# Kernel tuning notes

Hardware: AMD Instinct MI355X
Metric: run time of the kernel (lower is better)

Reference implementation:

```python
import jax, jax.numpy as jnp
import numpy as np

DN = ('NWC', 'WIO', 'NWC')  # Keras Conv1D layout: x=[B,T,C], w=[k,Cin,Cout]


def causal_conv(x, w, b, dilation):
    k = w.shape[0]
    pad = (k - 1) * dilation
    xp = jnp.pad(x, ((0, 0), (pad, 0), (0, 0)))
    y = jax.lax.conv_general_dilated(xp, w, window_strides=(1,), padding='VALID',
                                     rhs_dilation=(dilation,), dimension_numbers=DN)
    return jax.nn.relu(y + b)


def setup_inputs() -> dict:
    key = jax.random.key(0)
    ks = jax.random.split(key, 20)
    B, T, Cin, F = 32, 4096, 192, 320
    cb, cl = F // 5, F - 4 * (F // 5)  # 64, 64
    s = 0.05
    inp = {
        'x': jax.random.normal(ks[0], (B, T, Cin), jnp.float32),
        'w_b1': jax.random.normal(ks[1], (3, Cin, cb), jnp.float32) * s,
        'b_b1': jax.random.normal(ks[2], (cb,), jnp.float32) * s,
        'w_b2': jax.random.normal(ks[3], (3, Cin, cb), jnp.float32) * s,
        'b_b2': jax.random.normal(ks[4], (cb,), jnp.float32) * s,
        'w_b3': jax.random.normal(ks[5], (5, Cin, cb), jnp.float32) * s,
        'b_b3': jax.random.normal(ks[6], (cb,), jnp.float32) * s,
        'w_b4': jax.random.normal(ks[7], (9, Cin, cb), jnp.float32) * s,
        'b_b4': jax.random.normal(ks[8], (cb,), jnp.float32) * s,
        'w_b5': jax.random.normal(ks[9], (9, Cin, cl), jnp.float32) * s,
        'b_b5': jax.random.normal(ks[10], (cl,), jnp.float32) * s,
        'w_att1': jax.random.normal(ks[11], (F, F // 4), jnp.float32) * s,
        'b_att1': jax.random.normal(ks[12], (F // 4,), jnp.float32) * s,
        'w_att2': jax.random.normal(ks[13], (F // 4, F), jnp.float32) * s,
        'b_att2': jax.random.normal(ks[14], (F,), jnp.float32) * s,
        'w_out': jax.random.normal(ks[15], (1, F, F), jnp.float32) * s,
        'b_out': jax.random.normal(ks[16], (F,), jnp.float32) * s,
    }
    return inp


def reference(x, w_b1, b_b1, w_b2, b_b2, w_b3, b_b3, w_b4, b_b4, w_b5, b_b5,
              w_att1, b_att1, w_att2, b_att2, w_out, b_out):
    # multi-scale causal dilated branches (sequence-processing path)
    x1 = causal_conv(x, w_b1, b_b1, 1)
    x2 = causal_conv(x, w_b2, b_b2, 2)
    x3 = causal_conv(x, w_b3, b_b3, 4)
    x4 = causal_conv(x, w_b4, b_b4, 8)
    x5 = causal_conv(x, w_b5, b_b5, 12)
    xc = jnp.concatenate([x1, x2, x3, x4, x5], axis=-1)  # [B,T,F]
    # SE-style per-timestep gating
    att = jax.nn.relu(jnp.einsum('btf,fh->bth', xc, w_att1) + b_att1)
    att = jax.nn.sigmoid(jnp.einsum('bth,hf->btf', att, w_att2) + b_att2)
    xa = xc * att
    # 1x1 conv out == matmul over channel dim
    return jnp.einsum('btf,fg->btg', xa, w_out[0]) + b_out
```

## Files before the change

### kernel.cpp

```cpp
#include <hip/hip_runtime.h>

typedef __attribute__((ext_vector_type(8))) short short8;
typedef __attribute__((ext_vector_type(16))) float f32x16;
typedef __attribute__((ext_vector_type(4))) unsigned short us4;

#define MFMA32(a,b,c) __builtin_amdgcn_mfma_f32_32x32x16_bf16((a),(b),(c),0,0,0)

__device__ __forceinline__ unsigned short f2bf(float f) {
  union { float f; unsigned u; } v; v.f = f;
  return (unsigned short)((v.u + 0x7fffu + ((v.u >> 16) & 1u)) >> 16);
}
__device__ __forceinline__ float bf2f(unsigned short h) {
  union { unsigned u; float f; } v; v.u = ((unsigned)h) << 16;
  return v.f;
}
__device__ __forceinline__ f32x16 zero16() {
  f32x16 v;
  #pragma unroll
  for (int i = 0; i < 16; ++i) v[i] = 0.f;
  return v;
}

__global__ __launch_bounds__(256) void k_prep(
    const float* __restrict__ w1, const float* __restrict__ w2,
    const float* __restrict__ w3, const float* __restrict__ w4,
    const float* __restrict__ w5,
    const float* __restrict__ b1, const float* __restrict__ b2,
    const float* __restrict__ b3, const float* __restrict__ b4,
    const float* __restrict__ b5,
    const float* __restrict__ wa1, const float* __restrict__ wa2,
    const float* __restrict__ wo,
    unsigned short* __restrict__ wtcf, unsigned short* __restrict__ w1f,
    unsigned short* __restrict__ w2f, unsigned short* __restrict__ wof,
    float* __restrict__ bcat)
{
  int i = blockIdx.x * 256 + threadIdx.x;
  if (i < 356352) {
    int e = i & 7, l = (i >> 3) & 63, ks = (i >> 9) % 12;
    int rest = i / 6144; int nt2 = rest & 1, t = rest >> 1;
    int k = ks * 16 + (l >> 5) * 8 + e;
    int n = nt2 * 32 + (l & 31);
    const float* w; int j;
    if (t < 3)       { w = w1; j = t; }
    else if (t < 6)  { w = w2; j = t - 3; }
    else if (t < 11) { w = w3; j = t - 6; }
    else if (t < 20) { w = w4; j = t - 11; }
    else             { w = w5; j = t - 20; }
    wtcf[i] = f2bf(w[(j * 192 + k) * 64 + n]);
    return;
  }
  i -= 356352;
  if (i < 30720) {
    int e = i & 7, l = (i >> 3) & 63, ks = (i >> 9) % 20, nt = i / 10240;
    int h = nt * 32 + (l & 31), k = ks * 16 + (l >> 5) * 8 + e;
    w1f[i] = (h < 80) ? f2bf(wa1[k * 80 + h]) : (unsigned short)0;
    return;
  }
  i -= 30720;
  if (i < 30720) {
    int e = i & 7, l = (i >> 3) & 63, ks = (i >> 9) % 6, nt = i / 3072;
    int f = nt * 32 + (l & 31), k = ks * 16 + (l >> 5) * 8 + e;
    w2f[i] = (k < 80) ? f2bf(wa2[k * 320 + f]) : (unsigned short)0;
    return;
  }
  i -= 30720;
  if (i < 102400) {
    int e = i & 7, l = (i >> 3) & 63, ks = (i >> 9) % 20, nt = i / 10240;
    int g = nt * 32 + (l & 31), k = ks * 16 + (l >> 5) * 8 + e;
    wof[i] = f2bf(wo[k * 320 + g]);
    return;
  }
  i -= 102400;
  if (i < 320) {
    float v;
    if (i < 64)       v = b1[i];
    else if (i < 128) v = b2[i - 64];
    else if (i < 192) v = b3[i - 128];
    else if (i < 256) v = b4[i - 192];
    else              v = b5[i - 256];
    bcat[i] = v;
  }
}

#define XS_STRIDE 400
#define XCB_OFF   64000
#define LDS_TOTAL (64000 + 40960)

template<int KT, int DL, int TB>
__device__ __forceinline__ void conv_unit(
    const unsigned char* __restrict__ smem,
    unsigned char* __restrict__ xcb,
    const unsigned short* __restrict__ wtcf,
    const float* __restrict__ bcat,
    int br, int mt, int l31, int lh, int lane)
{
  f32x16 a0e = zero16(), a0o = zero16(), a1e = zero16(), a1o = zero16();
  const int arow0 = 96 + mt * 32 + l31;
  #pragma unroll
  for (int j = 0; j < KT; ++j) {
    const int roff = arow0 - DL * (KT - 1 - j);
    const unsigned char* xr = smem + roff * XS_STRIDE + lh * 16;
    const unsigned short* wp0 = wtcf + (size_t)((TB + j) * 2 + 0) * 6144 + lane * 8;
    const unsigned short* wp1 = wp0 + 6144;
    #pragma unroll
    for (int ks = 0; ks < 12; ks += 2) {
      short8 be0 = *(const short8*)(wp0 + ks * 512);
      short8 be1 = *(const short8*)(wp1 + ks * 512);
      short8 ae  = *(const short8*)(xr + ks * 32);
      a0e = MFMA32(ae, be0, a0e);
      a1e = MFMA32(ae, be1, a1e);
      short8 bo0 = *(const short8*)(wp0 + ks * 512 + 512);
      short8 bo1 = *(const short8*)(wp1 + ks * 512 + 512);
      short8 ao  = *(const short8*)(xr + ks * 32 + 32);
      a0o = MFMA32(ao, bo0, a0o);
      a1o = MFMA32(ao, bo1, a1o);
    }
  }
  #pragma unroll
  for (int nh = 0; nh < 2; ++nh) {
    const int col = (br * 2 + nh) * 32 + l31;
    const float bias = bcat[col];
    #pragma unroll
    for (int r = 0; r < 16; ++r) {
      int row = mt * 32 + (r & 3) + 8 * (r >> 2) + 4 * lh;
      float v = (nh ? (a1e[r] + a1o[r]) : (a0e[r] + a0o[r])) + bias;
      v = v > 0.f ? v : 0.f;
      *(unsigned short*)(xcb + row * 640 + ((2 * col) ^ ((row & 7) << 4))) = f2bf(v);
    }
  }
}

__global__ __launch_bounds__(512, 2) void k_fused(
    const float* __restrict__ x, const unsigned short* __restrict__ wtcf,
    const unsigned short* __restrict__ w1f, const unsigned short* __restrict__ w2f,
    const unsigned short* __restrict__ wof, const float* __restrict__ bcat,
    const float* __restrict__ ba1, const float* __restrict__ ba2,
    const float* __restrict__ bo, float* __restrict__ out)
{
  __shared__ __align__(16) unsigned char smem[LDS_TOTAL];
  unsigned char* xcb = smem + XCB_OFF;
  unsigned char* a1b = smem;

  int bid = blockIdx.x;
  bid = (bid & 7) * 256 + (bid >> 3);
  const int m0 = bid * 64;
  const int b  = m0 >> 12;
  const int t0 = m0 & 4095;
  const int tid = threadIdx.x;
  const int wid = tid >> 6, lane = tid & 63;
  const int l31 = lane & 31, lh = lane >> 5;
  const int sw = (l31 & 7) << 4;

  const float* xb = x + (size_t)b * 4096 * 192;
  #pragma unroll
  for (int it = 0; it < 15; ++it) {
    int c = tid + it * 512;
    int r = c / 48, f = c - r * 48;
    int tp = t0 - 96 + r;
    float4 v = make_float4(0.f, 0.f, 0.f, 0.f);
    if (tp >= 0) v = *(const float4*)(xb + (size_t)tp * 192 + f * 4);
    us4 o = { f2bf(v.x), f2bf(v.y), f2bf(v.z), f2bf(v.w) };
    *(us4*)(smem + r * XS_STRIDE + f * 8) = o;
  }
  __syncthreads();

  {
    const int mt = wid & 1;
    switch (wid >> 1) {
      case 0: conv_unit<9,12,20>(smem, xcb, wtcf, bcat, 4, mt, l31, lh, lane); break;
      case 1: conv_unit<9, 8,11>(smem, xcb, wtcf, bcat, 3, mt, l31, lh, lane); break;
      case 2: conv_unit<5, 4, 6>(smem, xcb, wtcf, bcat, 2, mt, l31, lh, lane); break;
      default:
        conv_unit<3, 2, 3>(smem, xcb, wtcf, bcat, 1, mt, l31, lh, lane);
        conv_unit<3, 1, 0>(smem, xcb, wtcf, bcat, 0, mt, l31, lh, lane);
        break;
    }
  }
  __syncthreads();

  if (wid < 6) {
    const int mt = wid & 1, nt1 = wid >> 1;
    const int arow = mt * 32 + l31;
    f32x16 acc = zero16();
    const unsigned short* bp = w1f + (size_t)(nt1 * 20) * 512 + lane * 8;
    #pragma unroll
    for (int ks = 0; ks < 20; ++ks) {
      short8 af = *(const short8*)(xcb + arow * 640 + ((ks * 32 + lh * 16) ^ sw));
      short8 bf = *(const short8*)(bp + ks * 512);
      acc = MFMA32(af, bf, acc);
    }
    const int h = nt1 * 32 + l31;
    const float bias = (h < 80) ? ba1[h] : 0.f;
    #pragma unroll
    for (int r = 0; r < 16; ++r) {
      int row = mt * 32 + (r & 3) + 8 * (r >> 2) + 4 * lh;
      float v = acc[r] + bias;
      v = v > 0.f ? v : 0.f;
      *(unsigned short*)(a1b + row * 256 + ((2 * h) ^ ((row & 7) << 4))) = f2bf(v);
    }
  }
  __syncthreads();

  const int mt2 = wid & 1, g = wid >> 1;
  const int tcount = (g < 2) ? 3 : 2;
  const int tbase  = (g < 2) ? g * 3 : 6 + (g - 2) * 2;
  const int arow2 = mt2 * 32 + l31;
  {
    f32x16 acc2[3];
    #pragma unroll
    for (int t = 0; t < 3; ++t) acc2[t] = zero16();
    #pragma unroll
    for (int ks = 0; ks < 6; ++ks) {
      short8 af = *(const short8*)(a1b + arow2 * 256 + ((ks * 32 + lh * 16) ^ sw));
      #pragma unroll
      for (int t = 0; t < 3; ++t) if (t < tcount) {
        short8 bf = *(const short8*)(w2f + (size_t)((tbase + t) * 6 + ks) * 512 + lane * 8);
        acc2[t] = MFMA32(af, bf, acc2[t]);
      }
    }
    #pragma unroll
    for (int t = 0; t < 3; ++t) if (t < tcount) {
      const int col = (tbase + t) * 32 + l31;
      const float bias = ba2[col];
      #pragma unroll
      for (int r = 0; r < 16; ++r) {
        int row = mt2 * 32 + (r & 3) + 8 * (r >> 2) + 4 * lh;
        float v = acc2[t][r] + bias;
        float s = 1.f / (1.f + __expf(-v));
        unsigned short* p =
            (unsigned short*)(xcb + row * 640 + ((2 * col) ^ ((row & 7) << 4)));
        *p = f2bf(bf2f(*p) * s);
      }
    }
  }
  __syncthreads();

  {
    f32x16 acc4[3];
    #pragma unroll
    for (int t = 0; t < 3; ++t) acc4[t] = zero16();
    #pragma unroll
    for (int ks = 0; ks < 20; ++ks) {
      short8 af = *(const short8*)(xcb + arow2 * 640 + ((ks * 32 + lh * 16) ^ sw));
      #pragma unroll
      for (int t = 0; t < 3; ++t) if (t < tcount) {
        short8 bf = *(const short8*)(wof + (size_t)((tbase + t) * 20 + ks) * 512 + lane * 8);
        acc4[t] = MFMA32(af, bf, acc4[t]);
      }
    }
    #pragma unroll
    for (int t = 0; t < 3; ++t) if (t < tcount) {
      const int col = (tbase + t) * 32 + l31;
      const float bias = bo[col];
      #pragma unroll
      for (int r = 0; r < 16; ++r) {
        int row = mt2 * 32 + (r & 3) + 8 * (r >> 2) + 4 * lh;
        out[(size_t)(m0 + row) * 320 + col] = acc4[t][r] + bias;
      }
    }
  }
}

extern "C" void kernel_launch(void* const* d_in, const int* in_sizes, int n_in,
                              void* d_out, int out_size, void* d_ws, size_t ws_size,
                              hipStream_t stream) {
  const float* x    = (const float*)d_in[0];
  const float* w_b1 = (const float*)d_in[1];  const float* b_b1 = (const float*)d_in[2];
  const float* w_b2 = (const float*)d_in[3];  const float* b_b2 = (const float*)d_in[4];
  const float* w_b3 = (const float*)d_in[5];  const float* b_b3 = (const float*)d_in[6];
  const float* w_b4 = (const float*)d_in[7];  const float* b_b4 = (const float*)d_in[8];
  const float* w_b5 = (const float*)d_in[9];  const float* b_b5 = (const float*)d_in[10];
  const float* wa1  = (const float*)d_in[11]; const float* ba1  = (const float*)d_in[12];
  const float* wa2  = (const float*)d_in[13]; const float* ba2  = (const float*)d_in[14];
  const float* wo   = (const float*)d_in[15]; const float* bo   = (const float*)d_in[16];

  char* ws = (char*)d_ws;
  unsigned short* wtcf = (unsigned short*)(ws);
  unsigned short* w1f  = (unsigned short*)(ws + 712704);
  unsigned short* w2f  = (unsigned short*)(ws + 774144);
  unsigned short* wof  = (unsigned short*)(ws + 835584);
  float*          bct  = (float*)         (ws + 1040384);

  k_prep<<<2034, 256, 0, stream>>>(w_b1, w_b2, w_b3, w_b4, w_b5,
                                   b_b1, b_b2, b_b3, b_b4, b_b5,
                                   wa1, wa2, wo, wtcf, w1f, w2f, wof, bct);
  k_fused<<<2048, 512, 0, stream>>>(x, wtcf, w1f, w2f, wof, bct,
                                    ba1, ba2, bo, (float*)d_out);
}
```

Before: 576.8 us.

## Split fused kernel into conv and gating/output kernels with 128-row tiles

Replaces the single fused kernel with two kernels. The first computes the five causal conv branches over 128-timestep tiles and writes the bf16 concatenated activations into the output buffer as scratch. The second stages that data into LDS with global_load_lds and then runs the SE gating and the output projection in place. Larger tiles shrink the relative halo cost and let each weight fragment feed two MFMAs, and the split frees LDS per stage. In exchange it adds a global round trip for the intermediate, and at 1024 threads per block with large LDS footprints occupancy is likely low.

Measured after the change: 492.9 us. -14.6%, faster.

```diff
diff --git a/kernel.cpp b/kernel.cpp
--- a/kernel.cpp
+++ b/kernel.cpp
@@ -19,6 +19,11 @@
   #pragma unroll
   for (int i = 0; i < 16; ++i) v[i] = 0.f;
   return v;
+}
+__device__ __forceinline__ void gload16(const void* g, void* l) {
+  __builtin_amdgcn_global_load_lds(
+      (const __attribute__((address_space(1))) void*)(g),
+      (__attribute__((address_space(3))) void*)(l), 16, 0, 0);
 }
 
 __global__ __launch_bounds__(256) void k_prep(
@@ -82,180 +87,183 @@
   }
 }
 
-#define XS_STRIDE 400
-#define XCB_OFF   64000
-#define LDS_TOTAL (64000 + 40960)
-
 template<int KT, int DL, int TB>
 __device__ __forceinline__ void conv_unit(
-    const unsigned char* __restrict__ smem,
-    unsigned char* __restrict__ xcb,
-    const unsigned short* __restrict__ wtcf,
-    const float* __restrict__ bcat,
-    int br, int mt, int l31, int lh, int lane)
-{
-  f32x16 a0e = zero16(), a0o = zero16(), a1e = zero16(), a1o = zero16();
-  const int arow0 = 96 + mt * 32 + l31;
+    const unsigned char* smem, const unsigned short* __restrict__ wtcf,
+    const float* __restrict__ bcat, unsigned char* __restrict__ xcg,
+    int nh, int p, int br, int l31, int lh, int lane)
+{
+  f32x16 acc0 = zero16(), acc1 = zero16();
+  const int r0 = 96 + p * 64 + l31;
   #pragma unroll
   for (int j = 0; j < KT; ++j) {
-    const int roff = arow0 - DL * (KT - 1 - j);
-    const unsigned char* xr = smem + roff * XS_STRIDE + lh * 16;
-    const unsigned short* wp0 = wtcf + (size_t)((TB + j) * 2 + 0) * 6144 + lane * 8;
-    const unsigned short* wp1 = wp0 + 6144;
-    #pragma unroll
-    for (int ks = 0; ks < 12; ks += 2) {
-      short8 be0 = *(const short8*)(wp0 + ks * 512);
-      short8 be1 = *(const short8*)(wp1 + ks * 512);
-      short8 ae  = *(const short8*)(xr + ks * 32);
-      a0e = MFMA32(ae, be0, a0e);
-      a1e = MFMA32(ae, be1, a1e);
-      short8 bo0 = *(const short8*)(wp0 + ks * 512 + 512);
-      short8 bo1 = *(const short8*)(wp1 + ks * 512 + 512);
-      short8 ao  = *(const short8*)(xr + ks * 32 + 32);
-      a0o = MFMA32(ao, bo0, a0o);
-      a1o = MFMA32(ao, bo1, a1o);
-    }
-  }
-  #pragma unroll
-  for (int nh = 0; nh < 2; ++nh) {
-    const int col = (br * 2 + nh) * 32 + l31;
-    const float bias = bcat[col];
+    const int row = r0 - DL * (KT - 1 - j);
+    const int sw = (row & 15) << 4;
+    const unsigned char* x0 = smem + row * 512;
+    const unsigned short* wp =
+        wtcf + (size_t)(((TB + j) * 2 + nh) * 12) * 512 + lane * 8;
+    #pragma unroll
+    for (int ks = 0; ks < 12; ++ks) {
+      const int cb = (ks * 32 + lh * 16) ^ sw;
+      short8 bf = *(const short8*)(wp + ks * 512);
+      short8 a0 = *(const short8*)(x0 + cb);
+      short8 a1 = *(const short8*)(x0 + 32 * 512 + cb);
+      acc0 = MFMA32(a0, bf, acc0);
+      acc1 = MFMA32(a1, bf, acc1);
+    }
+  }
+  const int col = (br * 2 + nh) * 32 + l31;
+  const float bias = bcat[col];
+  #pragma unroll
+  for (int h = 0; h < 2; ++h) {
+    const f32x16& A = h ? acc1 : acc0;
     #pragma unroll
     for (int r = 0; r < 16; ++r) {
-      int row = mt * 32 + (r & 3) + 8 * (r >> 2) + 4 * lh;
-      float v = (nh ? (a1e[r] + a1o[r]) : (a0e[r] + a0o[r])) + bias;
-      v = v > 0.f ? v : 0.f;
-      *(unsigned short*)(xcb + row * 640 + ((2 * col) ^ ((row & 7) << 4))) = f2bf(v);
-    }
-  }
-}
-
-__global__ __launch_bounds__(512, 2) void k_fused(
+      int row = p * 64 + h * 32 + (r & 3) + 8 * (r >> 2) + 4 * lh;
+      float v = A[r] + bias; v = v > 0.f ? v : 0.f;
+      *(unsigned short*)(xcg + (size_t)row * 768 +
+                         ((2 * col) ^ ((row & 15) << 4))) = f2bf(v);
+    }
+  }
+}
+
+__global__ __launch_bounds__(1024, 4) void k_fconv(
     const float* __restrict__ x, const unsigned short* __restrict__ wtcf,
-    const unsigned short* __restrict__ w1f, const unsigned short* __restrict__ w2f,
-    const unsigned short* __restrict__ wof, const float* __restrict__ bcat,
-    const float* __restrict__ ba1, const float* __restrict__ ba2,
-    const float* __restrict__ bo, float* __restrict__ out)
-{
-  __shared__ __align__(16) unsigned char smem[LDS_TOTAL];
-  unsigned char* xcb = smem + XCB_OFF;
-  unsigned char* a1b = smem;
-
+    const float* __restrict__ bcat, unsigned char* __restrict__ xcglob)
+{
+  __shared__ __align__(16) unsigned char smem[224 * 512];
   int bid = blockIdx.x;
-  bid = (bid & 7) * 256 + (bid >> 3);
-  const int m0 = bid * 64;
+  bid = (bid & 7) * 128 + (bid >> 3);
+  const int m0 = bid * 128;
   const int b  = m0 >> 12;
   const int t0 = m0 & 4095;
   const int tid = threadIdx.x;
+
+  const float* xb = x + (size_t)b * 4096 * 192;
+  #pragma unroll
+  for (int it = 0; it < 11; ++it) {
+    int c = tid + it * 1024;
+    if (c < 10752) {
+      int r = c / 48, f = c - r * 48;
+      int tp = t0 - 96 + r;
+      float4 v = make_float4(0.f, 0.f, 0.f, 0.f);
+      if (tp >= 0) v = *(const float4*)(xb + (size_t)tp * 192 + f * 4);
+      us4 o = { f2bf(v.x), f2bf(v.y), f2bf(v.z), f2bf(v.w) };
+      *(us4*)(smem + r * 512 + ((f * 8) ^ ((r & 15) << 4))) = o;
+    }
+  }
+  __syncthreads();
+
   const int wid = tid >> 6, lane = tid & 63;
   const int l31 = lane & 31, lh = lane >> 5;
-  const int sw = (l31 & 7) << 4;
-
-  const float* xb = x + (size_t)b * 4096 * 192;
-  #pragma unroll
-  for (int it = 0; it < 15; ++it) {
-    int c = tid + it * 512;
-    int r = c / 48, f = c - r * 48;
-    int tp = t0 - 96 + r;
-    float4 v = make_float4(0.f, 0.f, 0.f, 0.f);
-    if (tp >= 0) v = *(const float4*)(xb + (size_t)tp * 192 + f * 4);
-    us4 o = { f2bf(v.x), f2bf(v.y), f2bf(v.z), f2bf(v.w) };
-    *(us4*)(smem + r * XS_STRIDE + f * 8) = o;
-  }
-  __syncthreads();
+  unsigned char* xcg = xcglob + (size_t)m0 * 1280;
+
+  if (wid < 4)       conv_unit<9, 8,11>(smem, wtcf, bcat, xcg, (wid>>1)&1, wid&1, 3, l31, lh, lane);
+  else if (wid < 8)  conv_unit<9,12,20>(smem, wtcf, bcat, xcg, (wid>>1)&1, wid&1, 4, l31, lh, lane);
+  else if (wid < 12) conv_unit<5, 4, 6>(smem, wtcf, bcat, xcg, (wid>>1)&1, wid&1, 2, l31, lh, lane);
+  else if (wid < 14) {
+    conv_unit<3, 1, 0>(smem, wtcf, bcat, xcg, wid & 1, 0, 0, l31, lh, lane);
+    conv_unit<3, 1, 0>(smem, wtcf, bcat, xcg, wid & 1, 1, 0, l31, lh, lane);
+  } else {
+    conv_unit<3, 2, 3>(smem, wtcf, bcat, xcg, wid & 1, 0, 1, l31, lh, lane);
+    conv_unit<3, 2, 3>(smem, wtcf, bcat, xcg, wid & 1, 1, 1, l31, lh, lane);
+  }
+}
+
+__global__ __launch_bounds__(1024, 4) void k_gateout(
+    const unsigned char* __restrict__ xcglob,
+    const unsigned short* __restrict__ w1f, const unsigned short* __restrict__ w2f,
+    const unsigned short* __restrict__ wof,
+    const float* __restrict__ ba1, const float* __restrict__ ba2,
+    const float* __restrict__ bo, float* __restrict__ out)
+{
+  __shared__ __align__(16) unsigned char smem[128 * 768 + 128 * 256];
+  unsigned char* a1b = smem + 128 * 768;
+  int bid = blockIdx.x;
+  bid = (bid & 7) * 128 + (bid >> 3);
+  const int m0 = bid * 128;
+  const int tid = threadIdx.x;
+  const int wid = tid >> 6, lane = tid & 63;
+  const int l31 = lane & 31, lh = lane >> 5;
+  const int sw15 = (l31 & 15) << 4, sw7 = (l31 & 7) << 4;
 
   {
-    const int mt = wid & 1;
-    switch (wid >> 1) {
-      case 0: conv_unit<9,12,20>(smem, xcb, wtcf, bcat, 4, mt, l31, lh, lane); break;
-      case 1: conv_unit<9, 8,11>(smem, xcb, wtcf, bcat, 3, mt, l31, lh, lane); break;
-      case 2: conv_unit<5, 4, 6>(smem, xcb, wtcf, bcat, 2, mt, l31, lh, lane); break;
-      default:
-        conv_unit<3, 2, 3>(smem, xcb, wtcf, bcat, 1, mt, l31, lh, lane);
-        conv_unit<3, 1, 0>(smem, xcb, wtcf, bcat, 0, mt, l31, lh, lane);
-        break;
-    }
-  }
-  __syncthreads();
-
-  if (wid < 6) {
-    const int mt = wid & 1, nt1 = wid >> 1;
-    const int arow = mt * 32 + l31;
+    const unsigned char* src = xcglob + (size_t)m0 * 1280 + wid * 6144 + lane * 16;
+    unsigned char* dst = smem + wid * 6144;
+    #pragma unroll
+    for (int k = 0; k < 6; ++k)
+      gload16(src + k * 1024, dst + k * 1024);
+  }
+  __syncthreads();
+
+  if (wid < 12) {
+    const int nt = wid >> 2, mt = wid & 3;
     f32x16 acc = zero16();
-    const unsigned short* bp = w1f + (size_t)(nt1 * 20) * 512 + lane * 8;
+    const unsigned short* bp = w1f + (size_t)(nt * 20) * 512 + lane * 8;
+    const unsigned char* ar = smem + (size_t)(mt * 32 + l31) * 768;
     #pragma unroll
     for (int ks = 0; ks < 20; ++ks) {
-      short8 af = *(const short8*)(xcb + arow * 640 + ((ks * 32 + lh * 16) ^ sw));
+      short8 af = *(const short8*)(ar + ((ks * 32 + lh * 16) ^ sw15));
       short8 bf = *(const short8*)(bp + ks * 512);
       acc = MFMA32(af, bf, acc);
     }
-    const int h = nt1 * 32 + l31;
+    const int h = nt * 32 + l31;
     const float bias = (h < 80) ? ba1[h] : 0.f;
+    #pragma unroll
+    for (int r = 0; r < 16; ++r) {
+      int row = mt * 32 + (r & 3) + 8 * (r >> 2) + 4 * lh;
+      float v = acc[r] + bias; v = v > 0.f ? v : 0.f;
+      *(unsigned short*)(a1b + row * 256 + ((2 * h) ^ ((row & 7) << 4))) = f2bf(v);
+    }
+  }
+  __syncthreads();
+
+  for (int u = wid; u < 40; u += 16) {
+    const int col = u >> 2, mt = u & 3;
+    f32x16 acc = zero16();
+    const unsigned char* ar = a1b + (size_t)(mt * 32 + l31) * 256;
+    #pragma unroll
+    for (int ks = 0; ks < 6; ++ks) {
+      short8 af = *(const short8*)(ar + ((ks * 32 + lh * 16) ^ sw7));
+      short8 bf = *(const short8*)(w2f + (size_t)(col * 6 + ks) * 512 + lane * 8);
+      acc = MFMA32(af, bf, acc);
+    }
+    const float bias = ba2[col * 32 + l31];
     #pragma unroll
     for (int r = 0; r < 16; ++r) {
       int row = mt * 32 + (r & 3) + 8 * (r >> 2) + 4 * lh;
       float v = acc[r] + bias;
-      v = v > 0.f ? v : 0.f;
-      *(unsigned short*)(a1b + row * 256 + ((2 * h) ^ ((row & 7) << 4))) = f2bf(v);
-    }
-  }
-  __syncthreads();
-
-  const int mt2 = wid & 1, g = wid >> 1;
-  const int tcount = (g < 2) ? 3 : 2;
-  const int tbase  = (g < 2) ? g * 3 : 6 + (g - 2) * 2;
-  const int arow2 = mt2 * 32 + l31;
-  {
-    f32x16 acc2[3];
-    #pragma unroll
-    for (int t = 0; t < 3; ++t) acc2[t] = zero16();
-    #pragma unroll
-    for (int ks = 0; ks < 6; ++ks) {
-      short8 af = *(const short8*)(a1b + arow2 * 256 + ((ks * 32 + lh * 16) ^ sw));
-      #pragma unroll
-      for (int t = 0; t < 3; ++t) if (t < tcount) {
-        short8 bf = *(const short8*)(w2f + (size_t)((tbase + t) * 6 + ks) * 512 + lane * 8);
-        acc2[t] = MFMA32(af, bf, acc2[t]);
-      }
-    }
-    #pragma unroll
-    for (int t = 0; t < 3; ++t) if (t < tcount) {
-      const int col = (tbase + t) * 32 + l31;
-      const float bias = ba2[col];
+      float s = 1.f / (1.f + __expf(-v));
+      unsigned short* pp = (unsigned short*)(smem + (size_t)row * 768 +
+          ((2 * (col * 32 + l31)) ^ ((row & 15) << 4)));
+      *pp = f2bf(bf2f(*pp) * s);
+    }
+  }
+  __syncthreads();
+
+  for (int u = wid; u < 20; u += 16) {
+    const int col = u >> 1, p = u & 1;
+    f32x16 acc0 = zero16(), acc1 = zero16();
+    const unsigned char* ar0 = smem + (size_t)(p * 64 + l31) * 768;
+    const unsigned char* ar1 = ar0 + 32 * 768;
+    const unsigned short* bp = wof + (size_t)(col * 20) * 512 + lane * 8;
+    #pragma unroll
+    for (int ks = 0; ks < 20; ++ks) {
+      const int cb = (ks * 32 + lh * 16) ^ sw15;
+      short8 bf = *(const short8*)(bp + ks * 512);
+      short8 a0 = *(const short8*)(ar0 + cb);
+      short8 a1 = *(const short8*)(ar1 + cb);
+      acc0 = MFMA32(a0, bf, acc0);
+      acc1 = MFMA32(a1, bf, acc1);
+    }
+    const float bias = bo[col * 32 + l31];
+    #pragma unroll
+    for (int h = 0; h < 2; ++h) {
+      const f32x16& A = h ? acc1 : acc0;
       #pragma unroll
       for (int r = 0; r < 16; ++r) {
-        int row = mt2 * 32 + (r & 3) + 8 * (r >> 2) + 4 * lh;
-        float v = acc2[t][r] + bias;
-        float s = 1.f / (1.f + __expf(-v));
-        unsigned short* p =
-            (unsigned short*)(xcb + row * 640 + ((2 * col) ^ ((row & 7) << 4)));
-        *p = f2bf(bf2f(*p) * s);
-      }
-    }
-  }
-  __syncthreads();
-
-  {
-    f32x16 acc4[3];
-    #pragma unroll
-    for (int t = 0; t < 3; ++t) acc4[t] = zero16();
-    #pragma unroll
-    for (int ks = 0; ks < 20; ++ks) {
-      short8 af = *(const short8*)(xcb + arow2 * 640 + ((ks * 32 + lh * 16) ^ sw));
-      #pragma unroll
-      for (int t = 0; t < 3; ++t) if (t < tcount) {
-        short8 bf = *(const short8*)(wof + (size_t)((tbase + t) * 20 + ks) * 512 + lane * 8);
-        acc4[t] = MFMA32(af, bf, acc4[t]);
-      }
-    }
-    #pragma unroll
-    for (int t = 0; t < 3; ++t) if (t < tcount) {
-      const int col = (tbase + t) * 32 + l31;
-      const float bias = bo[col];
-      #pragma unroll
-      for (int r = 0; r < 16; ++r) {
-        int row = mt2 * 32 + (r & 3) + 8 * (r >> 2) + 4 * lh;
-        out[(size_t)(m0 + row) * 320 + col] = acc4[t][r] + bias;
+        int row = p * 64 + h * 32 + (r & 3) + 8 * (r >> 2) + 4 * lh;
+        out[(size_t)(m0 + row) * 320 + col * 32 + l31] = A[r] + bias;
       }
     }
   }
@@ -284,6 +292,8 @@
   k_prep<<<2034, 256, 0, stream>>>(w_b1, w_b2, w_b3, w_b4, w_b5,
                                    b_b1, b_b2, b_b3, b_b4, b_b5,
                                    wa1, wa2, wo, wtcf, w1f, w2f, wof, bct);
-  k_fused<<<2048, 512, 0, stream>>>(x, wtcf, w1f, w2f, wof, bct,
-                                    ba1, ba2, bo, (float*)d_out);
-}
+  k_fconv<<<1024, 1024, 0, stream>>>(x, wtcf, bct, (unsigned char*)d_out);
+  k_gateout<<<1024, 1024, 0, stream>>>((const unsigned char*)d_out,
+                                       w1f, w2f, wof, ba1, ba2, bo,
+                                       (float*)d_out);
+}
```

## Pre-pad x to bf16 in a separate pass and stream tiles via global_load_lds

Applied to the files above, without the earlier changes.

Adds a k_xpad kernel that converts x to bf16 with a 96-row causal zero pad and a padded row stride, so the fused kernel can copy its input tile straight into LDS with global_load_lds instead of converting per block. The conv stage is remapped so each wave computes both 32-row M tiles for one N half, reusing each weight register across two MFMAs, and epilogues are deferred until after a sync. LDS shrinks to about 66KB by reusing one buffer with padded strides in place of XOR swizzles, and launch bounds rise to 4 blocks per SM for higher occupancy. The cost is an extra full pass over x to and from global memory, plus possible LDS bank conflicts from the padded layout.

After: 498.2 us. 1.16x faster.

```diff
diff --git a/kernel.cpp b/kernel.cpp
--- a/kernel.cpp
+++ b/kernel.cpp
@@ -19,6 +19,11 @@
   #pragma unroll
   for (int i = 0; i < 16; ++i) v[i] = 0.f;
   return v;
+}
+__device__ __forceinline__ void gload16(const void* g, void* l) {
+  __builtin_amdgcn_global_load_lds(
+      (const __attribute__((address_space(1))) void*)(g),
+      (__attribute__((address_space(3))) void*)(l), 16, 0, 0);
 }
 
 __global__ __launch_bounds__(256) void k_prep(
@@ -82,65 +87,64 @@
   }
 }
 
-#define XS_STRIDE 400
-#define XCB_OFF   64000
-#define LDS_TOTAL (64000 + 40960)
+__global__ __launch_bounds__(256) void k_xpad(
+    const float* __restrict__ x, unsigned short* __restrict__ xpad)
+{
+  int i = blockIdx.x * 256 + threadIdx.x;
+  if (i >= 32 * 4192 * 50) return;
+  int c4 = i % 50; int rest = i / 50;
+  int r = rest % 4192; int b = rest / 4192;
+  us4 o = {0, 0, 0, 0};
+  if (r >= 96 && c4 < 48) {
+    float4 v = *(const float4*)(x + ((size_t)(b * 4096 + r - 96) * 192 + c4 * 4));
+    o[0] = f2bf(v.x); o[1] = f2bf(v.y); o[2] = f2bf(v.z); o[3] = f2bf(v.w);
+  }
+  *(us4*)(xpad + (size_t)(b * 4192 + r) * 200 + c4 * 4) = o;
+}
+
+#define XC_S 392
+#define A1_S 136
+#define A1_OFF 50176
 
 template<int KT, int DL, int TB>
 __device__ __forceinline__ void conv_unit(
-    const unsigned char* __restrict__ smem,
-    unsigned char* __restrict__ xcb,
+    const unsigned short* __restrict__ xsS,
     const unsigned short* __restrict__ wtcf,
-    const float* __restrict__ bcat,
-    int br, int mt, int l31, int lh, int lane)
+    int nh, int l31, int lh, int lane, f32x16& acc0, f32x16& acc1)
 {
-  f32x16 a0e = zero16(), a0o = zero16(), a1e = zero16(), a1o = zero16();
-  const int arow0 = 96 + mt * 32 + l31;
+  const int r0 = 96 + l31;
   #pragma unroll
   for (int j = 0; j < KT; ++j) {
-    const int roff = arow0 - DL * (KT - 1 - j);
-    const unsigned char* xr = smem + roff * XS_STRIDE + lh * 16;
-    const unsigned short* wp0 = wtcf + (size_t)((TB + j) * 2 + 0) * 6144 + lane * 8;
-    const unsigned short* wp1 = wp0 + 6144;
-    #pragma unroll
-    for (int ks = 0; ks < 12; ks += 2) {
-      short8 be0 = *(const short8*)(wp0 + ks * 512);
-      short8 be1 = *(const short8*)(wp1 + ks * 512);
-      short8 ae  = *(const short8*)(xr + ks * 32);
-      a0e = MFMA32(ae, be0, a0e);
-      a1e = MFMA32(ae, be1, a1e);
-      short8 bo0 = *(const short8*)(wp0 + ks * 512 + 512);
-      short8 bo1 = *(const short8*)(wp1 + ks * 512 + 512);
-      short8 ao  = *(const short8*)(xr + ks * 32 + 32);
-      a0o = MFMA32(ao, bo0, a0o);
-      a1o = MFMA32(ao, bo1, a1o);
-    }
-  }
-  #pragma unroll
-  for (int nh = 0; nh < 2; ++nh) {
-    const int col = (br * 2 + nh) * 32 + l31;
-    const float bias = bcat[col];
-    #pragma unroll
-    for (int r = 0; r < 16; ++r) {
-      int row = mt * 32 + (r & 3) + 8 * (r >> 2) + 4 * lh;
-      float v = (nh ? (a1e[r] + a1o[r]) : (a0e[r] + a0o[r])) + bias;
-      v = v > 0.f ? v : 0.f;
-      *(unsigned short*)(xcb + row * 640 + ((2 * col) ^ ((row & 7) << 4))) = f2bf(v);
-    }
-  }
-}
-
-__global__ __launch_bounds__(512, 2) void k_fused(
-    const float* __restrict__ x, const unsigned short* __restrict__ wtcf,
+    const int row = r0 - DL * (KT - 1 - j);
+    const unsigned short* xr = xsS + row * 200 + lh * 8;
+    const unsigned short* wp = wtcf + (size_t)((TB + j) * 2 + nh) * 6144 + lane * 8;
+    #pragma unroll
+    for (int half = 0; half < 2; ++half) {
+      short8 breg[6];
+      #pragma unroll
+      for (int ks = 0; ks < 6; ++ks)
+        breg[ks] = *(const short8*)(wp + (half * 6 + ks) * 512);
+      #pragma unroll
+      for (int ks = 0; ks < 6; ++ks) {
+        const int kk = half * 6 + ks;
+        short8 a0 = *(const short8*)(xr + kk * 16);
+        short8 a1 = *(const short8*)(xr + 32 * 200 + kk * 16);
+        acc0 = MFMA32(a0, breg[ks], acc0);
+        acc1 = MFMA32(a1, breg[ks], acc1);
+      }
+    }
+  }
+}
+
+__global__ __launch_bounds__(512, 4) void k_fused(
+    const unsigned short* __restrict__ xpad,
+    const unsigned short* __restrict__ wtcf,
     const unsigned short* __restrict__ w1f, const unsigned short* __restrict__ w2f,
     const unsigned short* __restrict__ wof, const float* __restrict__ bcat,
     const float* __restrict__ ba1, const float* __restrict__ ba2,
     const float* __restrict__ bo, float* __restrict__ out)
 {
-  __shared__ __align__(16) unsigned char smem[LDS_TOTAL];
-  unsigned char* xcb = smem + XCB_OFF;
-  unsigned char* a1b = smem;
-
+  __shared__ __align__(16) unsigned char smem[67584];
   int bid = blockIdx.x;
   bid = (bid & 7) * 256 + (bid >> 3);
   const int m0 = bid * 64;
@@ -149,86 +153,117 @@
   const int tid = threadIdx.x;
   const int wid = tid >> 6, lane = tid & 63;
   const int l31 = lane & 31, lh = lane >> 5;
-  const int sw = (l31 & 7) << 4;
-
-  const float* xb = x + (size_t)b * 4096 * 192;
-  #pragma unroll
-  for (int it = 0; it < 15; ++it) {
-    int c = tid + it * 512;
-    int r = c / 48, f = c - r * 48;
-    int tp = t0 - 96 + r;
-    float4 v = make_float4(0.f, 0.f, 0.f, 0.f);
-    if (tp >= 0) v = *(const float4*)(xb + (size_t)tp * 192 + f * 4);
-    us4 o = { f2bf(v.x), f2bf(v.y), f2bf(v.z), f2bf(v.w) };
-    *(us4*)(smem + r * XS_STRIDE + f * 8) = o;
-  }
-  __syncthreads();
-
-  {
-    const int mt = wid & 1;
+
+  {
+    const unsigned char* xsrc =
+        (const unsigned char*)(xpad + ((size_t)b * 4192 + t0) * 200);
+    #pragma unroll
+    for (int it = 0; it < 8; ++it) {
+      int off = (tid + it * 512) * 16;
+      gload16(xsrc + off, smem + off);
+    }
+  }
+  __syncthreads();
+
+  f32x16 c0a = zero16(), c0b = zero16(), c1a = zero16(), c1b = zero16();
+  const int nh = wid & 1;
+  {
+    const unsigned short* xsS = (const unsigned short*)smem;
     switch (wid >> 1) {
-      case 0: conv_unit<9,12,20>(smem, xcb, wtcf, bcat, 4, mt, l31, lh, lane); break;
-      case 1: conv_unit<9, 8,11>(smem, xcb, wtcf, bcat, 3, mt, l31, lh, lane); break;
-      case 2: conv_unit<5, 4, 6>(smem, xcb, wtcf, bcat, 2, mt, l31, lh, lane); break;
+      case 0: conv_unit<9,12,20>(xsS, wtcf, nh, l31, lh, lane, c0a, c0b); break;
+      case 1: conv_unit<9, 8,11>(xsS, wtcf, nh, l31, lh, lane, c0a, c0b); break;
+      case 2: conv_unit<5, 4, 6>(xsS, wtcf, nh, l31, lh, lane, c0a, c0b); break;
       default:
-        conv_unit<3, 2, 3>(smem, xcb, wtcf, bcat, 1, mt, l31, lh, lane);
-        conv_unit<3, 1, 0>(smem, xcb, wtcf, bcat, 0, mt, l31, lh, lane);
+        conv_unit<3, 2, 3>(xsS, wtcf, nh, l31, lh, lane, c0a, c0b);
+        conv_unit<3, 1, 0>(xsS, wtcf, nh, l31, lh, lane, c1a, c1b);
         break;
     }
   }
   __syncthreads();
 
+  {
+    unsigned short* xcS = (unsigned short*)smem;
+    const int brmap = (wid >> 1 == 0) ? 4 : (wid >> 1 == 1) ? 3 :
+                      (wid >> 1 == 2) ? 2 : 1;
+    const int col0 = (brmap * 2 + nh) * 32 + l31;
+    const float bias0 = bcat[col0];
+    #pragma unroll
+    for (int r = 0; r < 16; ++r) {
+      int row = (r & 3) + 8 * (r >> 2) + 4 * lh;
+      float v0 = c0a[r] + bias0; v0 = v0 > 0.f ? v0 : 0.f;
+      float v1 = c0b[r] + bias0; v1 = v1 > 0.f ? v1 : 0.f;
+      xcS[row * XC_S + col0]        = f2bf(v0);
+      xcS[(row + 32) * XC_S + col0] = f2bf(v1);
+    }
+    if ((wid >> 1) == 3) {
+      const int col1 = (0 * 2 + nh) * 32 + l31;
+      const float bias1 = bcat[col1];
+      #pragma unroll
+      for (int r = 0; r < 16; ++r) {
+        int row = (r & 3) + 8 * (r >> 2) + 4 * lh;
+        float v0 = c1a[r] + bias1; v0 = v0 > 0.f ? v0 : 0.f;
+        float v1 = c1b[r] + bias1; v1 = v1 > 0.f ? v1 : 0.f;
+        xcS[row * XC_S + col1]        = f2bf(v0);
+        xcS[(row + 32) * XC_S + col1] = f2bf(v1);
+      }
+    }
+  }
+  __syncthreads();
+
+  const unsigned short* xcS = (const unsigned short*)smem;
+  unsigned short* a1S = (unsigned short*)(smem + A1_OFF);
+
   if (wid < 6) {
-    const int mt = wid & 1, nt1 = wid >> 1;
-    const int arow = mt * 32 + l31;
+    const int nt = wid >> 1, mt = wid & 1;
     f32x16 acc = zero16();
-    const unsigned short* bp = w1f + (size_t)(nt1 * 20) * 512 + lane * 8;
+    const unsigned short* ar = xcS + (mt * 32 + l31) * XC_S + lh * 8;
+    const unsigned short* bp = w1f + (size_t)(nt * 20) * 512 + lane * 8;
     #pragma unroll
     for (int ks = 0; ks < 20; ++ks) {
-      short8 af = *(const short8*)(xcb + arow * 640 + ((ks * 32 + lh * 16) ^ sw));
+      short8 af = *(const short8*)(ar + ks * 16);
       short8 bf = *(const short8*)(bp + ks * 512);
       acc = MFMA32(af, bf, acc);
     }
-    const int h = nt1 * 32 + l31;
+    const int h = nt * 32 + l31;
     const float bias = (h < 80) ? ba1[h] : 0.f;
     #pragma unroll
     for (int r = 0; r < 16; ++r) {
       int row = mt * 32 + (r & 3) + 8 * (r >> 2) + 4 * lh;
-      float v = acc[r] + bias;
-      v = v > 0.f ? v : 0.f;
-      *(unsigned short*)(a1b + row * 256 + ((2 * h) ^ ((row & 7) << 4))) = f2bf(v);
-    }
-  }
-  __syncthreads();
-
-  const int mt2 = wid & 1, g = wid >> 1;
-  const int tcount = (g < 2) ? 3 : 2;
-  const int tbase  = (g < 2) ? g * 3 : 6 + (g - 2) * 2;
-  const int arow2 = mt2 * 32 + l31;
-  {
-    f32x16 acc2[3];
-    #pragma unroll
-    for (int t = 0; t < 3; ++t) acc2[t] = zero16();
+      float v = acc[r] + bias; v = v > 0.f ? v : 0.f;
+      a1S[row * A1_S + h] = f2bf(v);
+    }
+  }
+  __syncthreads();
+
+  const int mt2 = wid & 1, cw = wid >> 1;
+  {
+    f32x16 q0 = zero16(), q1 = zero16(), q2 = zero16();
+    const unsigned short* ar = a1S + (mt2 * 32 + l31) * A1_S + lh * 8;
     #pragma unroll
     for (int ks = 0; ks < 6; ++ks) {
-      short8 af = *(const short8*)(a1b + arow2 * 256 + ((ks * 32 + lh * 16) ^ sw));
-      #pragma unroll
-      for (int t = 0; t < 3; ++t) if (t < tcount) {
-        short8 bf = *(const short8*)(w2f + (size_t)((tbase + t) * 6 + ks) * 512 + lane * 8);
-        acc2[t] = MFMA32(af, bf, acc2[t]);
-      }
-    }
-    #pragma unroll
-    for (int t = 0; t < 3; ++t) if (t < tcount) {
-      const int col = (tbase + t) * 32 + l31;
-      const float bias = ba2[col];
+      short8 af = *(const short8*)(ar + ks * 16);
+      short8 b0 = *(const short8*)(w2f + (size_t)((cw    ) * 6 + ks) * 512 + lane * 8);
+      short8 b1 = *(const short8*)(w2f + (size_t)((cw + 4) * 6 + ks) * 512 + lane * 8);
+      q0 = MFMA32(af, b0, q0);
+      q1 = MFMA32(af, b1, q1);
+      if (cw < 2) {
+        short8 b2v = *(const short8*)(w2f + (size_t)((cw + 8) * 6 + ks) * 512 + lane * 8);
+        q2 = MFMA32(af, b2v, q2);
+      }
+    }
+    unsigned short* xcW = (unsigned short*)smem;
+    #pragma unroll
+    for (int t = 0; t < 3; ++t) {
+      if (t == 2 && cw >= 2) break;
+      const f32x16& Q = (t == 0) ? q0 : (t == 1) ? q1 : q2;
+      const int c = cw + 4 * t;
+      const float bias = ba2[c * 32 + l31];
       #pragma unroll
       for (int r = 0; r < 16; ++r) {
         int row = mt2 * 32 + (r & 3) + 8 * (r >> 2) + 4 * lh;
-        float v = acc2[t][r] + bias;
+        float v = Q[r] + bias;
         float s = 1.f / (1.f + __expf(-v));
-        unsigned short* p =
-            (unsigned short*)(xcb + row * 640 + ((2 * col) ^ ((row & 7) << 4)));
+        unsigned short* p = xcW + row * XC_S + c * 32 + l31;
         *p = f2bf(bf2f(*p) * s);
       }
     }
@@ -236,26 +271,30 @@
   __syncthreads();
 
   {
-    f32x16 acc4[3];
-    #pragma unroll
-    for (int t = 0; t < 3; ++t) acc4[t] = zero16();
+    f32x16 o0 = zero16(), o1 = zero16(), o2 = zero16();
+    const unsigned short* ar = xcS + (mt2 * 32 + l31) * XC_S + lh * 8;
     #pragma unroll
     for (int ks = 0; ks < 20; ++ks) {
-      short8 af = *(const short8*)(xcb + arow2 * 640 + ((ks * 32 + lh * 16) ^ sw));
-      #pragma unroll
-      for (int t = 0; t < 3; ++t) if (t < tcount) {
-        short8 bf = *(const short8*)(wof + (size_t)((tbase + t) * 20 + ks) * 512 + lane * 8);
-        acc4[t] = MFMA32(af, bf, acc4[t]);
-      }
-    }
-    #pragma unroll
-    for (int t = 0; t < 3; ++t) if (t < tcount) {
-      const int col = (tbase + t) * 32 + l31;
-      const float bias = bo[col];
+      short8 af = *(const short8*)(ar + ks * 16);
+      short8 b0 = *(const short8*)(wof + (size_t)((cw    ) * 20 + ks) * 512 + lane * 8);
+      short8 b1 = *(const short8*)(wof + (size_t)((cw + 4) * 20 + ks) * 512 + lane * 8);
+      o0 = MFMA32(af, b0, o0);
+      o1 = MFMA32(af, b1, o1);
+      if (cw < 2) {
+        short8 b2v = *(const short8*)(wof + (size_t)((cw + 8) * 20 + ks) * 512 + lane * 8);
+        o2 = MFMA32(af, b2v, o2);
+      }
+    }
+    #pragma unroll
+    for (int t = 0; t < 3; ++t) {
+      if (t == 2 && cw >= 2) break;
+      const f32x16& O = (t == 0) ? o0 : (t == 1) ? o1 : o2;
+      const int c = cw + 4 * t;
+      const float bias = bo[c * 32 + l31];
       #pragma unroll
       for (int r = 0; r < 16; ++r) {
         int row = mt2 * 32 + (r & 3) + 8 * (r >> 2) + 4 * lh;
-        out[(size_t)(m0 + row) * 320 + col] = acc4[t][r] + bias;
+        out[(size_t)(m0 + row) * 320 + c * 32 + l31] = O[r] + bias;
       }
     }
   }
@@ -280,10 +319,12 @@
   unsigned short* w2f  = (unsigned short*)(ws + 774144);
   unsigned short* wof  = (unsigned short*)(ws + 835584);
   float*          bct  = (float*)         (ws + 1040384);
+  unsigned short* xpad = (unsigned short*)(ws + 1041664);
 
   k_prep<<<2034, 256, 0, stream>>>(w_b1, w_b2, w_b3, w_b4, w_b5,
                                    b_b1, b_b2, b_b3, b_b4, b_b5,
                                    wa1, wa2, wo, wtcf, w1f, w2f, wof, bct);
-  k_fused<<<2048, 512, 0, stream>>>(x, wtcf, w1f, w2f, wof, bct,
+  k_xpad<<<26200, 256, 0, stream>>>(x, xpad);
+  k_fused<<<2048, 512, 0, stream>>>(xpad, wtcf, w1f, w2f, wof, bct,
                                     ba1, ba2, bo, (float*)d_out);
 }
```
